# Performance work log

Measured on AMD Instinct MI355X. Metric: run time of the kernel, lower is better.

The kernel has to match this reference:

```python
import jax, jax.numpy as jnp
import numpy as np

DK = 64

def setup_inputs() -> dict:
    key = jax.random.key(0)
    kx, kq, kk, kv = jax.random.split(key, 4)
    B, T, DM, DV = 256, 256, 384, 64
    x = jax.random.normal(kx, (B, T, DM), dtype=jnp.float32)
    s = 1.0 / np.sqrt(DM)
    W_q = jax.random.normal(kq, (DM, DK), dtype=jnp.float32) * s
    W_k = jax.random.normal(kk, (DM, DK), dtype=jnp.float32) * s
    W_v = jax.random.normal(kv, (DM, DV), dtype=jnp.float32) * s
    return {"x": x, "W_q": W_q, "W_k": W_k, "W_v": W_v}

def reference(x, W_q, W_k, W_v):
    # x: [B, T, dm]; projections to [B, T, dk]/[B, T, dv]
    q = jnp.einsum('btc,ck->btk', x, W_q)
    k = jnp.einsum('btc,ck->btk', x, W_k)
    v = jnp.einsum('btc,cv->btv', x, W_v)
    scale = k.shape[-1] ** (-0.5)
    wei = jnp.einsum('btk,bsk->bts', q, k) * scale  # [B, T, T]
    T = x.shape[1]
    causal = jnp.tril(jnp.ones((T, T), dtype=bool))
    wei = jnp.where(causal, wei, -jnp.inf)
    wei = jax.nn.softmax(wei, axis=-1)
    # dropout omitted (eval mode / deterministic reference)
    out = jnp.einsum('bts,bsv->btv', wei, v)
    return out
```

## Files before the change

### kernel.cpp

```cpp
#include <hip/hip_runtime.h>
#include <hip/hip_bf16.h>


typedef __attribute__((ext_vector_type(8))) short short8;
typedef __attribute__((ext_vector_type(4))) float floatx4;

__device__ inline unsigned short f2bf(float f) {
  union { float f; unsigned u; } v; v.f = f;
  unsigned r = v.u + 0x7FFFu + ((v.u >> 16) & 1u);
  return (unsigned short)(r >> 16);
}
__device__ inline unsigned pk2bf(float lo, float hi) {
  __hip_bfloat162 h = __float22bfloat162_rn(make_float2(lo, hi));
  union { __hip_bfloat162 h; unsigned u; } c; c.h = h;
  return c.u;
}

__device__ inline void glds16(const void* g, void* l) {
  __builtin_amdgcn_global_load_lds(
      (const __attribute__((address_space(1))) void*)g,
      (__attribute__((address_space(3))) void*)l, 16, 0, 0);
}

__global__ void wt_kernel(const float* __restrict__ wq, const float* __restrict__ wk,
                          const float* __restrict__ wv, unsigned short* __restrict__ wt) {
  int idx = blockIdx.x * 256 + threadIdx.x;
  if (idx >= 3 * 64 * 384) return;
  int mat = idx / (64 * 384);
  int rem = idx % (64 * 384);
  int n = rem / 384, k = rem % 384;
  const float* w = (mat == 0) ? wq : ((mat == 1) ? wk : wv);
  wt[idx] = f2bf(w[k * 64 + n]);
}

__global__ __launch_bounds__(1024) void fused_kernel(
    const float* __restrict__ x, const unsigned short* __restrict__ wt,
    float* __restrict__ out) {
  __shared__ __align__(16) unsigned char lds[147456];
  unsigned short* wtl = (unsigned short*)lds;
  unsigned short* sK  = (unsigned short*)lds;
  unsigned short* sVT = (unsigned short*)(lds + 36864);
  unsigned short* sQ  = (unsigned short*)(lds + 70656);
  unsigned short* scrA = (unsigned short*)(lds + 107520);

  int tid = threadIdx.x, lane = tid & 63, w = tid >> 6;
  int m = lane & 15, q = lane >> 4;
  int rg = w >> 1, cg = w & 1;
  int b = blockIdx.x;
  const float* xb = x + (size_t)b * 256 * 384;

#pragma unroll
  for (int t = 0; t < 9; ++t) {
    int i = w * 9 + t;
    int chunk = i / 12, sub = i % 12;
    int c = sub * 16 + (lane >> 2);
    int g = (lane & 3) ^ (c & 3);
    glds16(wt + (size_t)c * 384 + chunk * 32 + g * 8,
           (void*)(wtl + i * 512));
  }

  const float* arow0 = xb + (size_t)(32 * rg + m) * 384 + q * 8;
  const float* arow1 = arow0 + 16 * 384;
  float4 c00 = *(const float4*)arow0, c01 = *(const float4*)(arow0 + 4);
  float4 c10 = *(const float4*)arow1, c11 = *(const float4*)(arow1 + 4);

  floatx4 z = {0.f, 0.f, 0.f, 0.f};
  floatx4 acc[2][6];
#pragma unroll
  for (int a = 0; a < 2; ++a)
#pragma unroll
    for (int n = 0; n < 6; ++n) acc[a][n] = z;

  __syncthreads();

#pragma unroll 1
  for (int ks = 0; ks < 12; ++ks) {
    float4 n00, n01, n10, n11;
    if (ks < 11) {
      n00 = *(const float4*)(arow0 + (ks + 1) * 32);
      n01 = *(const float4*)(arow0 + (ks + 1) * 32 + 4);
      n10 = *(const float4*)(arow1 + (ks + 1) * 32);
      n11 = *(const float4*)(arow1 + (ks + 1) * 32 + 4);
    }
    short8 af[2];
    {
      union { short8 s; unsigned u[4]; } t0, t1;
      t0.u[0] = pk2bf(c00.x, c00.y); t0.u[1] = pk2bf(c00.z, c00.w);
      t0.u[2] = pk2bf(c01.x, c01.y); t0.u[3] = pk2bf(c01.z, c01.w);
      t1.u[0] = pk2bf(c10.x, c10.y); t1.u[1] = pk2bf(c10.z, c10.w);
      t1.u[2] = pk2bf(c11.x, c11.y); t1.u[3] = pk2bf(c11.z, c11.w);
      af[0] = t0.s; af[1] = t1.s;
    }
    const unsigned short* wck = wtl + ks * 6144;
#pragma unroll
    for (int nt = 0; nt < 6; ++nt) {
      int c = cg * 96 + nt * 16 + m;
      short8 bf = *(const short8*)&wck[c * 32 + (q ^ (m & 3)) * 8];
      acc[0][nt] = __builtin_amdgcn_mfma_f32_16x16x32_bf16(af[0], bf, acc[0][nt], 0, 0, 0);
      acc[1][nt] = __builtin_amdgcn_mfma_f32_16x16x32_bf16(af[1], bf, acc[1][nt], 0, 0, 0);
    }
    c00 = n00; c01 = n01; c10 = n10; c11 = n11;
  }

  __syncthreads();

#pragma unroll
  for (int mt = 0; mt < 2; ++mt) {
    int rowb = 32 * rg + mt * 16 + q * 4;
#pragma unroll
    for (int nt = 0; nt < 6; ++nt) {
      int cb = cg * 96 + nt * 16;
      if (cb < 128) {
#pragma unroll
        for (int j = 0; j < 4; ++j) {
          unsigned short val = f2bf(acc[mt][nt][j]);
          if (cb < 64) sQ[(rowb + j) * 72 + cb + m]      = val;
          else         sK[(rowb + j) * 72 + cb - 64 + m] = val;
        }
      } else {
        ushort4 pv;
        pv.x = f2bf(acc[mt][nt][0]); pv.y = f2bf(acc[mt][nt][1]);
        pv.z = f2bf(acc[mt][nt][2]); pv.w = f2bf(acc[mt][nt][3]);
        *(ushort4*)&sVT[(cb - 128 + m) * 264 + rowb] = pv;
      }
    }
  }

  __syncthreads();

  short8 qf0 = *(const short8*)(sQ + (w * 16 + m) * 72 + q * 8);
  short8 qf1 = *(const short8*)(sQ + (w * 16 + m) * 72 + 32 + q * 8);
  floatx4 sacc[16];
#pragma unroll
  for (int nt = 0; nt < 16; ++nt) {
    if (nt > w) continue;
    short8 kb0 = *(const short8*)(sK + (nt * 16 + m) * 72 + q * 8);
    short8 kb1 = *(const short8*)(sK + (nt * 16 + m) * 72 + 32 + q * 8);
    floatx4 t = __builtin_amdgcn_mfma_f32_16x16x32_bf16(qf0, kb0, z, 0, 0, 0);
    sacc[nt] = __builtin_amdgcn_mfma_f32_16x16x32_bf16(qf1, kb1, t, 0, 0, 0);
  }

  const float CSC = 0.18033688011112042f;
  float inv_[4];
  int rbase = w * 16 + q * 4;
#pragma unroll
  for (int j = 0; j < 4; ++j) {
    int rgl = rbase + j;
    float sum = 0.f;
#pragma unroll
    for (int nt = 0; nt < 16; ++nt) {
      if (nt > w) continue;
      int col = nt * 16 + m;
      float p = (col <= rgl) ? exp2f(sacc[nt][j] * CSC) : 0.f;
      sacc[nt][j] = p;
      sum += p;
    }
    sum += __shfl_xor(sum, 1);
    sum += __shfl_xor(sum, 2);
    sum += __shfl_xor(sum, 4);
    sum += __shfl_xor(sum, 8);
    inv_[j] = 1.f / sum;
  }

  unsigned short* scr = scrA + w * 1152;
  floatx4 o[4];
#pragma unroll
  for (int vt = 0; vt < 4; ++vt) o[vt] = z;
#pragma unroll
  for (int c = 0; c < 4; ++c) {
    if (4 * c > w) continue;
#pragma unroll
    for (int t = 0; t < 4; ++t) {
      int nt = 4 * c + t;
#pragma unroll
      for (int j = 0; j < 4; ++j) {
        unsigned short pv = (nt <= w) ? f2bf(sacc[nt][j] * inv_[j]) : (unsigned short)0;
        scr[(q * 4 + j) * 72 + t * 16 + m] = pv;
      }
    }
    short8 pf0 = *(const short8*)(scr + m * 72 + q * 8);
    short8 pf1 = *(const short8*)(scr + m * 72 + 32 + q * 8);
#pragma unroll
    for (int vt = 0; vt < 4; ++vt) {
      short8 vb0 = *(const short8*)(sVT + (vt * 16 + m) * 264 + c * 64 + q * 8);
      short8 vb1 = *(const short8*)(sVT + (vt * 16 + m) * 264 + c * 64 + 32 + q * 8);
      o[vt] = __builtin_amdgcn_mfma_f32_16x16x32_bf16(pf0, vb0, o[vt], 0, 0, 0);
      o[vt] = __builtin_amdgcn_mfma_f32_16x16x32_bf16(pf1, vb1, o[vt], 0, 0, 0);
    }
  }

  float* op = out + ((size_t)b * 256 + w * 16) * 64;
#pragma unroll
  for (int vt = 0; vt < 4; ++vt)
#pragma unroll
    for (int j = 0; j < 4; ++j)
      op[(q * 4 + j) * 64 + vt * 16 + m] = o[vt][j];
}

extern "C" void kernel_launch(void* const* d_in, const int* in_sizes, int n_in,
                              void* d_out, int out_size, void* d_ws, size_t ws_size,
                              hipStream_t stream) {
  const float* x  = (const float*)d_in[0];
  const float* wq = (const float*)d_in[1];
  const float* wk = (const float*)d_in[2];
  const float* wv = (const float*)d_in[3];
  float* out = (float*)d_out;

  unsigned short* wt = (unsigned short*)d_ws;

  wt_kernel<<<288, 256, 0, stream>>>(wq, wk, wv, wt);
  fused_kernel<<<256, 1024, 0, stream>>>(x, wt, out);
}
```

Baseline: 176.2 us.

## Split fused attention into separate QKV projection and attention kernels

```diff
diff --git a/kernel.cpp b/kernel.cpp
--- a/kernel.cpp
+++ b/kernel.cpp
@@ -14,12 +14,6 @@
   __hip_bfloat162 h = __float22bfloat162_rn(make_float2(lo, hi));
   union { __hip_bfloat162 h; unsigned u; } c; c.h = h;
   return c.u;
-}
-
-__device__ inline void glds16(const void* g, void* l) {
-  __builtin_amdgcn_global_load_lds(
-      (const __attribute__((address_space(1))) void*)g,
-      (__attribute__((address_space(3))) void*)l, 16, 0, 0);
 }
 
 __global__ void wt_kernel(const float* __restrict__ wq, const float* __restrict__ wk,
@@ -33,123 +27,121 @@
   wt[idx] = f2bf(w[k * 64 + n]);
 }
 
-__global__ __launch_bounds__(1024) void fused_kernel(
+__global__ __launch_bounds__(256) void qkv_kernel(
     const float* __restrict__ x, const unsigned short* __restrict__ wt,
-    float* __restrict__ out) {
-  __shared__ __align__(16) unsigned char lds[147456];
-  unsigned short* wtl = (unsigned short*)lds;
-  unsigned short* sK  = (unsigned short*)lds;
-  unsigned short* sVT = (unsigned short*)(lds + 36864);
-  unsigned short* sQ  = (unsigned short*)(lds + 70656);
-  unsigned short* scrA = (unsigned short*)(lds + 107520);
+    unsigned short* __restrict__ q, unsigned short* __restrict__ kk,
+    unsigned short* __restrict__ vt) {
+  __shared__ __align__(16) unsigned short vtile[64 * 40];
 
   int tid = threadIdx.x, lane = tid & 63, w = tid >> 6;
-  int m = lane & 15, q = lane >> 4;
+  int m = lane & 15, qd = lane >> 4;
   int rg = w >> 1, cg = w & 1;
-  int b = blockIdx.x;
-  const float* xb = x + (size_t)b * 256 * 384;
-
-#pragma unroll
-  for (int t = 0; t < 9; ++t) {
-    int i = w * 9 + t;
-    int chunk = i / 12, sub = i % 12;
-    int c = sub * 16 + (lane >> 2);
-    int g = (lane & 3) ^ (c & 3);
-    glds16(wt + (size_t)c * 384 + chunk * 32 + g * 8,
-           (void*)(wtl + i * 512));
-  }
-
-  const float* arow0 = xb + (size_t)(32 * rg + m) * 384 + q * 8;
-  const float* arow1 = arow0 + 16 * 384;
-  float4 c00 = *(const float4*)arow0, c01 = *(const float4*)(arow0 + 4);
-  float4 c10 = *(const float4*)arow1, c11 = *(const float4*)(arow1 + 4);
+  int tok0 = blockIdx.x * 32;
+  int row = tok0 + rg * 16 + m;
+
+  const float* arow = x + (size_t)row * 384 + qd * 8;
 
   floatx4 z = {0.f, 0.f, 0.f, 0.f};
-  floatx4 acc[2][6];
-#pragma unroll
-  for (int a = 0; a < 2; ++a)
-#pragma unroll
-    for (int n = 0; n < 6; ++n) acc[a][n] = z;
-
-  __syncthreads();
+  floatx4 acc[6];
+#pragma unroll
+  for (int nt = 0; nt < 6; ++nt) acc[nt] = z;
+
+  float4 c0 = *(const float4*)arow;
+  float4 c1 = *(const float4*)(arow + 4);
 
 #pragma unroll 1
   for (int ks = 0; ks < 12; ++ks) {
-    float4 n00, n01, n10, n11;
+    float4 n0, n1;
     if (ks < 11) {
-      n00 = *(const float4*)(arow0 + (ks + 1) * 32);
-      n01 = *(const float4*)(arow0 + (ks + 1) * 32 + 4);
-      n10 = *(const float4*)(arow1 + (ks + 1) * 32);
-      n11 = *(const float4*)(arow1 + (ks + 1) * 32 + 4);
-    }
-    short8 af[2];
+      n0 = *(const float4*)(arow + (ks + 1) * 32);
+      n1 = *(const float4*)(arow + (ks + 1) * 32 + 4);
+    }
+    short8 af;
     {
-      union { short8 s; unsigned u[4]; } t0, t1;
-      t0.u[0] = pk2bf(c00.x, c00.y); t0.u[1] = pk2bf(c00.z, c00.w);
-      t0.u[2] = pk2bf(c01.x, c01.y); t0.u[3] = pk2bf(c01.z, c01.w);
-      t1.u[0] = pk2bf(c10.x, c10.y); t1.u[1] = pk2bf(c10.z, c10.w);
-      t1.u[2] = pk2bf(c11.x, c11.y); t1.u[3] = pk2bf(c11.z, c11.w);
-      af[0] = t0.s; af[1] = t1.s;
-    }
-    const unsigned short* wck = wtl + ks * 6144;
+      union { short8 s; unsigned u[4]; } t;
+      t.u[0] = pk2bf(c0.x, c0.y); t.u[1] = pk2bf(c0.z, c0.w);
+      t.u[2] = pk2bf(c1.x, c1.y); t.u[3] = pk2bf(c1.z, c1.w);
+      af = t.s;
+    }
 #pragma unroll
     for (int nt = 0; nt < 6; ++nt) {
       int c = cg * 96 + nt * 16 + m;
-      short8 bf = *(const short8*)&wck[c * 32 + (q ^ (m & 3)) * 8];
-      acc[0][nt] = __builtin_amdgcn_mfma_f32_16x16x32_bf16(af[0], bf, acc[0][nt], 0, 0, 0);
-      acc[1][nt] = __builtin_amdgcn_mfma_f32_16x16x32_bf16(af[1], bf, acc[1][nt], 0, 0, 0);
-    }
-    c00 = n00; c01 = n01; c10 = n10; c11 = n11;
+      short8 bf = *(const short8*)&wt[(size_t)c * 384 + ks * 32 + qd * 8];
+      acc[nt] = __builtin_amdgcn_mfma_f32_16x16x32_bf16(af, bf, acc[nt], 0, 0, 0);
+    }
+    c0 = n0; c1 = n1;
+  }
+
+#pragma unroll
+  for (int nt = 0; nt < 6; ++nt) {
+    int cb = cg * 96 + nt * 16;
+    int rowb = tok0 + rg * 16 + qd * 4;
+    if (cb < 64) {
+#pragma unroll
+      for (int j = 0; j < 4; ++j)
+        q[(size_t)(rowb + j) * 64 + cb + m] = f2bf(acc[nt][j]);
+    } else if (cb < 128) {
+#pragma unroll
+      for (int j = 0; j < 4; ++j)
+        kk[(size_t)(rowb + j) * 64 + cb - 64 + m] = f2bf(acc[nt][j]);
+    } else {
+      ushort4 pv;
+      pv.x = f2bf(acc[nt][0]); pv.y = f2bf(acc[nt][1]);
+      pv.z = f2bf(acc[nt][2]); pv.w = f2bf(acc[nt][3]);
+      *(ushort4*)&vtile[(cb - 128 + m) * 40 + rg * 16 + qd * 4] = pv;
+    }
   }
 
   __syncthreads();
-
-#pragma unroll
-  for (int mt = 0; mt < 2; ++mt) {
-    int rowb = 32 * rg + mt * 16 + q * 4;
-#pragma unroll
-    for (int nt = 0; nt < 6; ++nt) {
-      int cb = cg * 96 + nt * 16;
-      if (cb < 128) {
-#pragma unroll
-        for (int j = 0; j < 4; ++j) {
-          unsigned short val = f2bf(acc[mt][nt][j]);
-          if (cb < 64) sQ[(rowb + j) * 72 + cb + m]      = val;
-          else         sK[(rowb + j) * 72 + cb - 64 + m] = val;
-        }
-      } else {
-        ushort4 pv;
-        pv.x = f2bf(acc[mt][nt][0]); pv.y = f2bf(acc[mt][nt][1]);
-        pv.z = f2bf(acc[mt][nt][2]); pv.w = f2bf(acc[mt][nt][3]);
-        *(ushort4*)&sVT[(cb - 128 + m) * 264 + rowb] = pv;
-      }
-    }
-  }
-
-  __syncthreads();
-
-  short8 qf0 = *(const short8*)(sQ + (w * 16 + m) * 72 + q * 8);
-  short8 qf1 = *(const short8*)(sQ + (w * 16 + m) * 72 + 32 + q * 8);
+  {
+    int col = tid >> 2, sg = tid & 3;
+    int b = tok0 >> 8, tm = tok0 & 255;
+    uint4 d = *(const uint4*)&vtile[col * 40 + sg * 8];
+    *(uint4*)&vt[((size_t)b * 64 + col) * 256 + tm + sg * 8] = d;
+  }
+}
+
+__global__ __launch_bounds__(256) void attn_kernel(
+    const unsigned short* __restrict__ Q, const unsigned short* __restrict__ K,
+    const unsigned short* __restrict__ Vt, float* __restrict__ out) {
+  __shared__ __align__(16) unsigned short scrA[4 * 1152];
+
+  int tid = threadIdx.x, lane = tid & 63, wv = tid >> 6;
+  int m = lane & 15, qd = lane >> 4;
+  int b = blockIdx.x >> 2, qt = blockIdx.x & 3;
+  int W = qt * 4 + wv;
+  int r0 = W * 16;
+
+  const unsigned short* Qg = Q + ((size_t)b * 256 + r0 + m) * 64;
+  const unsigned short* Kg = K + (size_t)b * 256 * 64;
+  const unsigned short* Vg = Vt + (size_t)b * 64 * 256;
+
+  short8 qf0 = *(const short8*)&Qg[qd * 8];
+  short8 qf1 = *(const short8*)&Qg[32 + qd * 8];
+
+  floatx4 z = {0.f, 0.f, 0.f, 0.f};
   floatx4 sacc[16];
+
 #pragma unroll
   for (int nt = 0; nt < 16; ++nt) {
-    if (nt > w) continue;
-    short8 kb0 = *(const short8*)(sK + (nt * 16 + m) * 72 + q * 8);
-    short8 kb1 = *(const short8*)(sK + (nt * 16 + m) * 72 + 32 + q * 8);
+    if (nt > W) continue;
+    const unsigned short* kr = Kg + (size_t)(nt * 16 + m) * 64;
+    short8 kb0 = *(const short8*)&kr[qd * 8];
+    short8 kb1 = *(const short8*)&kr[32 + qd * 8];
     floatx4 t = __builtin_amdgcn_mfma_f32_16x16x32_bf16(qf0, kb0, z, 0, 0, 0);
     sacc[nt] = __builtin_amdgcn_mfma_f32_16x16x32_bf16(qf1, kb1, t, 0, 0, 0);
   }
 
   const float CSC = 0.18033688011112042f;
   float inv_[4];
-  int rbase = w * 16 + q * 4;
+  int rbase = r0 + qd * 4;
 #pragma unroll
   for (int j = 0; j < 4; ++j) {
     int rgl = rbase + j;
     float sum = 0.f;
 #pragma unroll
     for (int nt = 0; nt < 16; ++nt) {
-      if (nt > w) continue;
+      if (nt > W) continue;
       int col = nt * 16 + m;
       float p = (col <= rgl) ? exp2f(sacc[nt][j] * CSC) : 0.f;
       sacc[nt][j] = p;
@@ -162,39 +154,40 @@
     inv_[j] = 1.f / sum;
   }
 
-  unsigned short* scr = scrA + w * 1152;
+  unsigned short* scr = scrA + wv * 1152;
   floatx4 o[4];
 #pragma unroll
-  for (int vt = 0; vt < 4; ++vt) o[vt] = z;
+  for (int vtl = 0; vtl < 4; ++vtl) o[vtl] = z;
 #pragma unroll
   for (int c = 0; c < 4; ++c) {
-    if (4 * c > w) continue;
+    if (4 * c > W) continue;
 #pragma unroll
     for (int t = 0; t < 4; ++t) {
       int nt = 4 * c + t;
 #pragma unroll
       for (int j = 0; j < 4; ++j) {
-        unsigned short pv = (nt <= w) ? f2bf(sacc[nt][j] * inv_[j]) : (unsigned short)0;
-        scr[(q * 4 + j) * 72 + t * 16 + m] = pv;
+        unsigned short pv = (nt <= W) ? f2bf(sacc[nt][j] * inv_[j]) : (unsigned short)0;
+        scr[(qd * 4 + j) * 72 + t * 16 + m] = pv;
       }
     }
-    short8 pf0 = *(const short8*)(scr + m * 72 + q * 8);
-    short8 pf1 = *(const short8*)(scr + m * 72 + 32 + q * 8);
-#pragma unroll
-    for (int vt = 0; vt < 4; ++vt) {
-      short8 vb0 = *(const short8*)(sVT + (vt * 16 + m) * 264 + c * 64 + q * 8);
-      short8 vb1 = *(const short8*)(sVT + (vt * 16 + m) * 264 + c * 64 + 32 + q * 8);
-      o[vt] = __builtin_amdgcn_mfma_f32_16x16x32_bf16(pf0, vb0, o[vt], 0, 0, 0);
-      o[vt] = __builtin_amdgcn_mfma_f32_16x16x32_bf16(pf1, vb1, o[vt], 0, 0, 0);
-    }
-  }
-
-  float* op = out + ((size_t)b * 256 + w * 16) * 64;
-#pragma unroll
-  for (int vt = 0; vt < 4; ++vt)
+    short8 pf0 = *(const short8*)(scr + m * 72 + qd * 8);
+    short8 pf1 = *(const short8*)(scr + m * 72 + 32 + qd * 8);
+#pragma unroll
+    for (int vtl = 0; vtl < 4; ++vtl) {
+      const unsigned short* vr = Vg + (size_t)(vtl * 16 + m) * 256 + c * 64;
+      short8 vb0 = *(const short8*)&vr[qd * 8];
+      short8 vb1 = *(const short8*)&vr[32 + qd * 8];
+      o[vtl] = __builtin_amdgcn_mfma_f32_16x16x32_bf16(pf0, vb0, o[vtl], 0, 0, 0);
+      o[vtl] = __builtin_amdgcn_mfma_f32_16x16x32_bf16(pf1, vb1, o[vtl], 0, 0, 0);
+    }
+  }
+
+  float* op = out + ((size_t)b * 256 + r0) * 64;
+#pragma unroll
+  for (int vtl = 0; vtl < 4; ++vtl)
 #pragma unroll
     for (int j = 0; j < 4; ++j)
-      op[(q * 4 + j) * 64 + vt * 16 + m] = o[vt][j];
+      op[(qd * 4 + j) * 64 + vtl * 16 + m] = o[vtl][j];
 }
 
 extern "C" void kernel_launch(void* const* d_in, const int* in_sizes, int n_in,
@@ -207,7 +200,11 @@
   float* out = (float*)d_out;
 
   unsigned short* wt = (unsigned short*)d_ws;
+  unsigned short* q  = (unsigned short*)((char*)d_ws + 147456);
+  unsigned short* k  = q + (size_t)65536 * 64;
+  unsigned short* vt = k + (size_t)65536 * 64;
 
   wt_kernel<<<288, 256, 0, stream>>>(wq, wk, wv, wt);
-  fused_kernel<<<256, 1024, 0, stream>>>(x, wt, out);
-}
+  qkv_kernel<<<2048, 256, 0, stream>>>(x, wt, q, k, vt);
+  attn_kernel<<<1024, 256, 0, stream>>>(q, k, vt, out);
+}
```

New measurement: 277.2 us. 57.3% more time.
